# Kernel tuning notes

Hardware: AMD Instinct MI355X
Metric: run time of the kernel (lower is better)

Reference implementation:

```python
import jax, jax.numpy as jnp
import numpy as np

# Config matching init_kwargs: N=4 networks, dims 128 -> 1024 -> 1024 -> 512
A, B, D = 8, 2048, 128     # agents, batch, input size
N = 4                       # number of independent SePS networks
H1, H2, H3 = 1024, 1024, 512


def setup_inputs() -> dict:
    key = jax.random.key(0)
    ks = jax.random.split(key, 6)
    inputs = jax.random.normal(ks[0], (A, B, D), dtype=jnp.float32)  # stacked per-agent obs
    seps_indices = jax.random.randint(ks[1], (B, A), 0, N)           # cluster id per (sample, agent)
    scale = lambda k, shape, fan: jax.random.normal(k, shape, dtype=jnp.float32) * (1.0 / np.sqrt(fan))
    W0 = scale(ks[2], (N, D, H1), D);   b0 = jnp.zeros((N, H1), jnp.float32)
    W1 = scale(ks[3], (N, H1, H2), H1); b1 = jnp.zeros((N, H2), jnp.float32)
    W2 = scale(ks[4], (N, H2, H3), H2); b2 = jnp.zeros((N, H3), jnp.float32)
    return {"inputs": inputs, "seps_indices": seps_indices,
            "W0": W0, "b0": b0, "W1": W1, "b1": b1, "W2": W2, "b2": b2}


def reference(inputs, seps_indices, W0, b0, W1, b1, W2, b2):
    # Run every network densely on the full stacked input, as the torch module does.
    # inputs: [A, B, D]; W*: [N, in, out]
    h = jax.nn.relu(jnp.einsum('abd,ndh->nabh', inputs, W0) + b0[:, None, None, :])
    h = jax.nn.relu(jnp.einsum('nabh,nhk->nabk', h, W1) + b1[:, None, None, :])
    out_all = jnp.einsum('nabk,nko->nabo', h, W2) + b2[:, None, None, :]  # [N, A, B, H3]
    # Gather along the network axis per (agent, sample): seps_indices is [B, A]
    idx = seps_indices.T                              # [A, B]
    a = jnp.arange(inputs.shape[0])[:, None]          # [A, 1]
    b = jnp.arange(inputs.shape[1])[None, :]          # [1, B]
    return out_all[idx, a, b, :]                      # [A, B, H3] (stacked per-agent outputs)
```

## Files before the change

### kernel.cpp

```cpp
#include <hip/hip_runtime.h>
#include <hip/hip_bf16.h>

#define AG 8
#define BT 2048
#define RT (AG*BT)
#define NNET 4
#define D0 128
#define H1 1024
#define H2 1024
#define H3 512

#define XBLK 40

typedef __attribute__((ext_vector_type(8))) short short8;
typedef __attribute__((ext_vector_type(4))) float f32x4;

__device__ __forceinline__ unsigned short f2bf(float f){
  unsigned int x = __float_as_uint(f);
  x += 0x7fff + ((x >> 16) & 1);
  return (unsigned short)(x >> 16);
}

template<int N> __device__ __forceinline__ void vmw(){
  if constexpr (N==8)      asm volatile("s_waitcnt vmcnt(8)" ::: "memory");
  else if constexpr (N==4) asm volatile("s_waitcnt vmcnt(4)" ::: "memory");
  else                     asm volatile("s_waitcnt vmcnt(0)" ::: "memory");
}

__device__ __forceinline__ void gload_lds16(const void* g, void* l){
  __builtin_amdgcn_global_load_lds(
      (const __attribute__((address_space(1))) unsigned int*)g,
      (__attribute__((address_space(3))) unsigned int*)l, 16, 0, 0);
}

__device__ __forceinline__ int bucket_off(const int* counts, int n){
  int s = 0;
  #pragma unroll
  for (int i = 0; i < NNET-1; i++) if (i < n) s += counts[i];
  return s;
}

__global__ void k_init(int* counts){
  if (threadIdx.x < NNET) counts[threadIdx.x] = 0;
}

__global__ __launch_bounds__(256) void k_compact(const int* __restrict__ seps,
                          int* __restrict__ counts, int* __restrict__ rowlist){
  __shared__ int lcount[NNET];
  __shared__ int lbase[NNET];
  int t = blockIdx.x * 256 + threadIdx.x;
  if (threadIdx.x < NNET) lcount[threadIdx.x] = 0;
  __syncthreads();
  int a = t >> 11, b = t & (BT-1);
  int n = seps[b*AG + a];
  int lrank = atomicAdd(&lcount[n], 1);
  __syncthreads();
  if (threadIdx.x < NNET)
    lbase[threadIdx.x] = atomicAdd(&counts[threadIdx.x], lcount[threadIdx.x]);
  __syncthreads();
  rowlist[n*RT + lbase[n] + lrank] = t;
}

template<int K, int NOUT>
__global__ __launch_bounds__(256) void k_transpose(const float* __restrict__ W,
                                                   unsigned short* __restrict__ WT){
  __shared__ float tile[32][33];
  int n = blockIdx.z;
  int k0 = blockIdx.x*32, o0 = blockIdx.y*32;
  const float* Wn = W + (size_t)n*K*NOUT;
  unsigned short* WTn = WT + (size_t)n*NOUT*K;
  int tx = threadIdx.x & 31, ty0 = threadIdx.x >> 5;
  #pragma unroll
  for (int r = 0; r < 32; r += 8)
    tile[ty0 + r][tx] = Wn[(size_t)(k0 + ty0 + r)*NOUT + o0 + tx];
  __syncthreads();
  #pragma unroll
  for (int r = 0; r < 32; r += 8)
    WTn[(size_t)(o0 + ty0 + r)*K + k0 + tx] = f2bf(tile[tx][ty0 + r]);
}

__global__ __launch_bounds__(256) void k_gather0(const float* __restrict__ X,
                          const int* __restrict__ counts,
                          const int* __restrict__ rowlist, unsigned short* __restrict__ X0h){
  int n = blockIdx.y;
  int cnt = counts[n];
  int i = blockIdx.x*16 + (threadIdx.x >> 4);
  if (i >= cnt) return;
  int off = bucket_off(counts, n);
  int orig = rowlist[n*RT + i];
  int c = (threadIdx.x & 15) * 8;
  const float* src = X + (size_t)orig*D0 + c;
  float4 v0 = *(const float4*)src, v1 = *(const float4*)(src+4);
  ushort4 u0, u1;
  u0.x=f2bf(v0.x); u0.y=f2bf(v0.y); u0.z=f2bf(v0.z); u0.w=f2bf(v0.w);
  u1.x=f2bf(v1.x); u1.y=f2bf(v1.y); u1.z=f2bf(v1.z); u1.w=f2bf(v1.w);
  unsigned short* dst = X0h + (size_t)(off + i)*D0 + c;
  *(ushort4*)dst = u0; *(ushort4*)(dst+4) = u1;
}

template<int K, int NOUT, int RELU, int SCATTER, int PIN>
__global__ __launch_bounds__(256, 2) void k_mlp(
    const unsigned short* __restrict__ X,
    const unsigned short* __restrict__ WT,
    const float* __restrict__ Bias,
    const int* __restrict__ counts,
    const int* __restrict__ rowlist,
    unsigned short* __restrict__ Yh,
    float* __restrict__ Yf)
{
  constexpr int T = K / 32;
  const int n = blockIdx.z;
  const int cnt = counts[n];
  const int i0 = blockIdx.x * 128;
  if (i0 >= cnt) return;
  const int off = bucket_off(counts, n);
  const int bn = blockIdx.y * 128;

  __shared__ __align__(16) unsigned short As[3][128*32];
  __shared__ __align__(16) unsigned short Bs[3][128*32];
  __shared__ int rs[128];

  const int t = threadIdx.x, lane = t & 63, wave = t >> 6;
  const int wm = wave >> 1, wn = wave & 1;
  const int lr = lane & 15, g = lane >> 4;

  if (SCATTER && t < 128) rs[t] = rowlist[n*RT + min(i0 + t, cnt-1)];

  const unsigned short* pA[2]; const unsigned short* pB[2];
  unsigned int ldsoff[2];
  const unsigned short* WTn = WT + (size_t)n * NOUT * K;
  #pragma unroll
  for (int j = 0; j < 2; j++){
    int r  = (j*4 + wave)*16 + (lane >> 2);
    int ps = lane & 3;
    int ls = ps ^ ((r >> 1) & 3);
    int rA = min(i0 + r, cnt-1);
    pA[j] = X   + (size_t)(off + rA)*K + ls*8;
    pB[j] = WTn + (size_t)(bn  + r )*K + ls*8;
    ldsoff[j] = (unsigned)(j*4 + wave) * 512;
  }

  int aoff[4], boff[4];
  #pragma unroll
  for (int i = 0; i < 4; i++){
    int ra = wm*64 + i*16 + lr;
    aoff[i] = ra*32 + (g ^ ((ra>>1)&3))*8;
    int rb = wn*64 + i*16 + lr;
    boff[i] = rb*32 + (g ^ ((rb>>1)&3))*8;
  }

  __syncthreads();

  #pragma unroll
  for (int s = 0; s < 3; ++s){
    #pragma unroll
    for (int j = 0; j < 2; j++){
      gload_lds16(pA[j], &As[s][ldsoff[j]]);
      gload_lds16(pB[j], &Bs[s][ldsoff[j]]);
      pA[j] += 32; pB[j] += 32;
    }
  }

  f32x4 acc[4][4] = {};
  int b = 0;
  for (int ks = 0; ks < T; ++ks){
    if (ks < T-2)       vmw<8>();
    else if (ks == T-2) vmw<4>();
    else                vmw<0>();
    __builtin_amdgcn_s_barrier();

    short8 av[4], bv[4];
    #pragma unroll
    for (int i = 0; i < 4; i++) av[i] = *(const short8*)&As[b][aoff[i]];
    #pragma unroll
    for (int i = 0; i < 4; i++) bv[i] = *(const short8*)&Bs[b][boff[i]];

    if constexpr (PIN){
      asm volatile("s_waitcnt lgkmcnt(0)" ::: "memory");
      __builtin_amdgcn_sched_barrier(0);
      __builtin_amdgcn_s_barrier();
      if (ks + 3 < T){
        #pragma unroll
        for (int j = 0; j < 2; j++){
          gload_lds16(pA[j], &As[b][ldsoff[j]]);
          gload_lds16(pB[j], &Bs[b][ldsoff[j]]);
          pA[j] += 32; pB[j] += 32;
        }
      }
      __builtin_amdgcn_s_setprio(1);
      #pragma unroll
      for (int mi = 0; mi < 4; mi++)
        #pragma unroll
        for (int ni = 0; ni < 4; ni++)
          acc[mi][ni] = __builtin_amdgcn_mfma_f32_16x16x32_bf16(bv[ni], av[mi], acc[mi][ni], 0, 0, 0);
      __builtin_amdgcn_s_setprio(0);
    } else {
      #pragma unroll
      for (int mi = 0; mi < 4; mi++)
        #pragma unroll
        for (int ni = 0; ni < 4; ni++)
          acc[mi][ni] = __builtin_amdgcn_mfma_f32_16x16x32_bf16(bv[ni], av[mi], acc[mi][ni], 0, 0, 0);
      asm volatile("s_waitcnt lgkmcnt(0)" ::: "memory");
      __builtin_amdgcn_s_barrier();
      if (ks + 3 < T){
        #pragma unroll
        for (int j = 0; j < 2; j++){
          gload_lds16(pA[j], &As[b][ldsoff[j]]);
          gload_lds16(pB[j], &Bs[b][ldsoff[j]]);
          pA[j] += 32; pB[j] += 32;
        }
      }
    }

    b = (b == 2) ? 0 : b + 1;
  }

  f32x4 bias4[4];
  #pragma unroll
  for (int ni = 0; ni < 4; ni++)
    bias4[ni] = *(const f32x4*)&Bias[n*NOUT + bn + wn*64 + ni*16 + (g<<2)];

  #pragma unroll
  for (int mi = 0; mi < 4; mi++){
    int rloc = wm*64 + mi*16 + lr;
    int grow = i0 + rloc;
    if (grow < cnt){
      #pragma unroll
      for (int ni = 0; ni < 4; ni++){
        float o[4];
        #pragma unroll
        for (int i = 0; i < 4; i++){
          float v = acc[mi][ni][i] + bias4[ni][i];
          if (RELU) v = fmaxf(v, 0.f);
          o[i] = v;
        }
        int cb = bn + wn*64 + ni*16 + (g<<2);
        if (SCATTER){
          *(float4*)&Yf[(size_t)rs[rloc]*NOUT + cb] = make_float4(o[0],o[1],o[2],o[3]);
        } else {
          ushort4 u;
          u.x=f2bf(o[0]); u.y=f2bf(o[1]); u.z=f2bf(o[2]); u.w=f2bf(o[3]);
          *(ushort4*)&Yh[(size_t)(off + grow)*NOUT + cb] = u;
        }
      }
    }
  }
}

extern "C" void kernel_launch(void* const* d_in, const int* in_sizes, int n_in,
                              void* d_out, int out_size, void* d_ws, size_t ws_size,
                              hipStream_t stream) {
  const float* inputs = (const float*)d_in[0];
  const int*   seps   = (const int*)  d_in[1];
  const float* W0     = (const float*)d_in[2];
  const float* b0     = (const float*)d_in[3];
  const float* W1     = (const float*)d_in[4];
  const float* b1     = (const float*)d_in[5];
  const float* W2     = (const float*)d_in[6];
  const float* b2     = (const float*)d_in[7];
  float* out = (float*)d_out;

  char* ws = (char*)d_ws;
  int* counts  = (int*)ws;
  int* rowlist = (int*)(ws + 4096);
  const size_t MB = 1u << 20;
  unsigned short* WT0 = (unsigned short*)(ws + 1*MB);
  unsigned short* WT1 = (unsigned short*)(ws + 2*MB);
  unsigned short* WT2 = (unsigned short*)(ws + 10*MB);
  unsigned short* h1  = (unsigned short*)(ws + 14*MB);
  unsigned short* h2  = (unsigned short*)(ws + 46*MB);
  unsigned short* X0h = (unsigned short*)(ws + 46*MB);

  k_init   <<<1, 64, 0, stream>>>(counts);
  k_compact<<<RT/256, 256, 0, stream>>>(seps, counts, rowlist);

  k_transpose<D0, H1><<<dim3(D0/32, H1/32, NNET), 256, 0, stream>>>(W0, WT0);
  k_transpose<H1, H2><<<dim3(H1/32, H2/32, NNET), 256, 0, stream>>>(W1, WT1);
  k_transpose<H2, H3><<<dim3(H2/32, H3/32, NNET), 256, 0, stream>>>(W2, WT2);
  k_gather0<<<dim3(RT/16, NNET), 256, 0, stream>>>(inputs, counts, rowlist, X0h);

  k_mlp<D0, H1, 1, 0, 0><<<dim3(XBLK, H1/128, NNET), 256, 0, stream>>>(
      X0h, WT0, b0, counts, rowlist, h1, nullptr);
  k_mlp<H1, H2, 1, 0, 0><<<dim3(XBLK, H2/128, NNET), 256, 0, stream>>>(
      h1, WT1, b1, counts, rowlist, h2, nullptr);
  k_mlp<H2, H3, 0, 1, 1><<<dim3(XBLK, H3/128, NNET), 256, 0, stream>>>(
      h2, WT2, b2, counts, rowlist, nullptr, out);
}
```

Measured before the change: 133.7 us.

## Use 256x256-tile 8-wave GEMM kernel for the middle MLP layer

Adds a new k_mlp8 kernel with 512 threads, 256x256 output tiles, triple-buffered LDS and split A/B prefetch interleaved with two MFMA half-phases, and uses it for the 1024x1024 hidden layer. Larger tiles raise arithmetic intensity and cut global/LDS traffic per FLOP. The costs are fewer blocks (20x4x4), so CUs may sit underused and tail effects grow, plus higher register pressure with 128 accumulator values per thread.

```diff
diff --git a/kernel.cpp b/kernel.cpp
--- a/kernel.cpp
+++ b/kernel.cpp
@@ -11,6 +11,7 @@
 #define H3 512
 
 #define XBLK 40
+#define XBLK8 20
 
 typedef __attribute__((ext_vector_type(8))) short short8;
 typedef __attribute__((ext_vector_type(4))) float f32x4;
@@ -211,7 +212,6 @@
         }
       }
     }
-
     b = (b == 2) ? 0 : b + 1;
   }
 
@@ -247,6 +247,145 @@
   }
 }
 
+template<int K, int NOUT, int RELU>
+__global__ __launch_bounds__(512, 1) void k_mlp8(
+    const unsigned short* __restrict__ X,
+    const unsigned short* __restrict__ WT,
+    const float* __restrict__ Bias,
+    const int* __restrict__ counts,
+    unsigned short* __restrict__ Yh)
+{
+  constexpr int T = K / 32;
+  const int n = blockIdx.z;
+  const int cnt = counts[n];
+  const int i0 = blockIdx.x * 256;
+  if (i0 >= cnt) return;
+  const int off = bucket_off(counts, n);
+  const int bn = blockIdx.y * 256;
+
+  __shared__ __align__(16) unsigned short As[3][256*32];
+  __shared__ __align__(16) unsigned short Bs[3][256*32];
+
+  const int t = threadIdx.x, lane = t & 63;
+  const int wave = t >> 6;
+  const int wm = wave >> 2, wn = wave & 3;
+  const int lr = lane & 15, g = lane >> 4;
+
+  const unsigned short* pA[2]; const unsigned short* pB[2];
+  unsigned int loffA[2], loffB[2];
+  const unsigned short* WTn = WT + (size_t)n * NOUT * K;
+  #pragma unroll
+  for (int j = 0; j < 2; j++){
+    int s = j*512 + t, r = s >> 2;
+    int ls = (s & 3) ^ ((r >> 1) & 3);
+    pA[j] = X   + (size_t)(off + min(i0 + r, cnt-1))*K + ls*8;
+    pB[j] = WTn + (size_t)(bn + r)*K + ls*8;
+    loffA[j] = (unsigned)s * 8;
+    loffB[j] = (unsigned)s * 8;
+  }
+
+  int aoff[8], boff[4];
+  #pragma unroll
+  for (int i = 0; i < 8; i++){
+    int ra = wm*128 + i*16 + lr;
+    aoff[i] = ra*32 + (g ^ ((ra>>1)&3))*8;
+  }
+  #pragma unroll
+  for (int i = 0; i < 4; i++){
+    int rb = wn*64 + i*16 + lr;
+    boff[i] = rb*32 + (g ^ ((rb>>1)&3))*8;
+  }
+
+  __syncthreads();
+
+  #pragma unroll
+  for (int s = 0; s < 2; ++s){
+    #pragma unroll
+    for (int j = 0; j < 2; j++){
+      gload_lds16(pA[j], &As[s][loffA[j]]);
+      gload_lds16(pB[j], &Bs[s][loffB[j]]);
+      pA[j] += 32; pB[j] += 32;
+    }
+  }
+
+  f32x4 acc[8][4] = {};
+  short8 bv[4];
+  int b = 0, d = 2;
+  for (int s = 0; s < T; ++s){
+    if (s < T-1) vmw<4>(); else vmw<0>();
+    asm volatile("s_waitcnt lgkmcnt(0)" ::: "memory");
+    __builtin_amdgcn_s_barrier();
+    __builtin_amdgcn_sched_barrier(0);
+
+    if (s + 2 < T){
+      #pragma unroll
+      for (int j = 0; j < 2; j++){ gload_lds16(pA[j], &As[d][loffA[j]]); pA[j] += 32; }
+    }
+    {
+      short8 av[4];
+      #pragma unroll
+      for (int i = 0; i < 4; i++) av[i] = *(const short8*)&As[b][aoff[i]];
+      #pragma unroll
+      for (int i = 0; i < 4; i++) bv[i] = *(const short8*)&Bs[b][boff[i]];
+      __builtin_amdgcn_s_setprio(1);
+      #pragma unroll
+      for (int mi = 0; mi < 4; mi++)
+        #pragma unroll
+        for (int ni = 0; ni < 4; ni++)
+          acc[mi][ni] = __builtin_amdgcn_mfma_f32_16x16x32_bf16(bv[ni], av[mi], acc[mi][ni], 0, 0, 0);
+      __builtin_amdgcn_s_setprio(0);
+    }
+
+    __builtin_amdgcn_s_barrier();
+    if (s + 2 < T){
+      #pragma unroll
+      for (int j = 0; j < 2; j++){ gload_lds16(pB[j], &Bs[d][loffB[j]]); pB[j] += 32; }
+    }
+    {
+      short8 av[4];
+      #pragma unroll
+      for (int i = 0; i < 4; i++) av[i] = *(const short8*)&As[b][aoff[4+i]];
+      __builtin_amdgcn_s_setprio(1);
+      #pragma unroll
+      for (int mi = 0; mi < 4; mi++)
+        #pragma unroll
+        for (int ni = 0; ni < 4; ni++)
+          acc[4+mi][ni] = __builtin_amdgcn_mfma_f32_16x16x32_bf16(bv[ni], av[mi], acc[4+mi][ni], 0, 0, 0);
+      __builtin_amdgcn_s_setprio(0);
+    }
+
+    b = (b == 2) ? 0 : b + 1;
+    d = (d == 2) ? 0 : d + 1;
+  }
+
+  f32x4 bias4[4];
+  #pragma unroll
+  for (int ni = 0; ni < 4; ni++)
+    bias4[ni] = *(const f32x4*)&Bias[n*NOUT + bn + wn*64 + ni*16 + (g<<2)];
+
+  #pragma unroll
+  for (int mi = 0; mi < 8; mi++){
+    int rloc = wm*128 + mi*16 + lr;
+    int grow = i0 + rloc;
+    if (grow < cnt){
+      #pragma unroll
+      for (int ni = 0; ni < 4; ni++){
+        float o[4];
+        #pragma unroll
+        for (int i = 0; i < 4; i++){
+          float v = acc[mi][ni][i] + bias4[ni][i];
+          if (RELU) v = fmaxf(v, 0.f);
+          o[i] = v;
+        }
+        int cb = bn + wn*64 + ni*16 + (g<<2);
+        ushort4 u;
+        u.x=f2bf(o[0]); u.y=f2bf(o[1]); u.z=f2bf(o[2]); u.w=f2bf(o[3]);
+        *(ushort4*)&Yh[(size_t)(off + grow)*NOUT + cb] = u;
+      }
+    }
+  }
+}
+
 extern "C" void kernel_launch(void* const* d_in, const int* in_sizes, int n_in,
                               void* d_out, int out_size, void* d_ws, size_t ws_size,
                               hipStream_t stream) {
@@ -281,8 +420,8 @@
 
   k_mlp<D0, H1, 1, 0, 0><<<dim3(XBLK, H1/128, NNET), 256, 0, stream>>>(
       X0h, WT0, b0, counts, rowlist, h1, nullptr);
-  k_mlp<H1, H2, 1, 0, 0><<<dim3(XBLK, H2/128, NNET), 256, 0, stream>>>(
-      h1, WT1, b1, counts, rowlist, h2, nullptr);
+  k_mlp8<H1, H2, 1><<<dim3(XBLK8, H2/256, NNET), 512, 0, stream>>>(
+      h1, WT1, b1, counts, h2);
   k_mlp<H2, H3, 0, 1, 1><<<dim3(XBLK, H3/128, NNET), 256, 0, stream>>>(
       h2, WT2, b2, counts, rowlist, nullptr, out);
 }
```

Result: slower. 158.0 us (+18.1%).
